# Kernel optimization log

Hardware: AMD Instinct MI355X
Metric: run time of the kernel (lower is better)

The kernel has to match this reference:

```python
import jax, jax.numpy as jnp
import numpy as np

B, DIM, HID = 16384, 1024, 2048
HALF = DIM // 2
# alternating checkerboard mask: even indices are 'masked' (conditioning) dims
_MASK = np.arange(DIM) % 2 == 0
MASK_IDX = np.nonzero(_MASK)[0]      # dims fed to the MLP (static)
NEG_IDX = np.nonzero(~_MASK)[0]      # dims transformed by the affine coupling (static)


def setup_inputs() -> dict:
    key = jax.random.key(0)
    ks = jax.random.split(key, 8)
    s = 0.02  # small init so exp(s) stays well-behaved
    return {
        "z": jax.random.normal(ks[0], (B, DIM), jnp.float32),
        "log_det": jnp.zeros((B,), jnp.float32),
        "W1": jax.random.normal(ks[1], (HID, HALF), jnp.float32) * s,
        "b1": jax.random.normal(ks[2], (HID,), jnp.float32) * s,
        "W2": jax.random.normal(ks[3], (HID, HID), jnp.float32) * s,
        "b2": jax.random.normal(ks[4], (HID,), jnp.float32) * s,
        "W3": jax.random.normal(ks[5], (DIM, HID), jnp.float32) * s,
        "b3": jax.random.normal(ks[6], (DIM,), jnp.float32) * s,
    }


def reference(z, log_det, W1, b1, W2, b2, W3, b3):
    # gather conditioning dims (static column indices -> jit-friendly)
    zm = z[:, MASK_IDX]                                    # [B, HALF]
    # 3-layer MLP with exact (erf) GELU, matching torch nn.GELU default
    h = jax.nn.gelu(zm @ W1.T + b1, approximate=False)     # [B, HID]
    h = jax.nn.gelu(h @ W2.T + b2, approximate=False)      # [B, HID]
    s_t = h @ W3.T + b3                                    # [B, DIM]
    s, t = s_t[:, :HALF], s_t[:, HALF:]                    # each [B, HALF]
    # affine coupling on the complementary dims, scatter back (forward, inverse=False)
    z_out = z.at[:, NEG_IDX].set(z[:, NEG_IDX] * jnp.exp(s) + t)
    log_det_out = log_det + jnp.sum(s, axis=1)
    return z_out, log_det_out
```

## Files before the change

### kernel.cpp

```cpp
#include <hip/hip_runtime.h>
#include <hip/hip_bf16.h>
#include <cstdint>

typedef __bf16 bf16x8 __attribute__((ext_vector_type(8)));
typedef float  f32x4  __attribute__((ext_vector_type(4)));

struct alignas(4) us2 { unsigned short x, y; };
struct alignas(8) us4 { unsigned short x, y, z, w; };

__device__ __forceinline__ unsigned short f2bf(float f) {
    union { float f; unsigned u; } a; a.f = f;
    unsigned r = a.u + 0x7fffu + ((a.u >> 16) & 1u);
    return (unsigned short)(r >> 16);
}

__device__ __forceinline__ void gl_lds16(const void* g, void* s) {
    __builtin_amdgcn_global_load_lds(
        (const __attribute__((address_space(1))) void*)g,
        (__attribute__((address_space(3))) void*)s, 16, 0, 0);
}

#define SCHEDB()  __builtin_amdgcn_sched_barrier(0)
#define SBAR()    do { SCHEDB(); __builtin_amdgcn_s_barrier(); SCHEDB(); } while (0)
#define WAITLG(N) do { asm volatile("s_waitcnt lgkmcnt(" #N ")" ::: "memory"); SCHEDB(); } while (0)
#define WAITVM(N) do { asm volatile("s_waitcnt vmcnt(" #N ")" ::: "memory"); SCHEDB(); } while (0)

template<int EPI, int K, int N>
__global__ __launch_bounds__(512, 2)
void gemm256(const unsigned short* __restrict__ A,
             const unsigned short* __restrict__ W,
             const float* __restrict__ bias,
             unsigned short* __restrict__ outb,
             float* __restrict__ outf,
             const float* __restrict__ zin,
             float* __restrict__ ldout)
{
    extern __shared__ char smem[];
    constexpr int NH = K / 32;
    constexpr int GX = N / 256;

    const int tid  = threadIdx.x;
    const int lane = tid & 63;
    const int wv   = tid >> 6;
    const int wr   = wv >> 2, wc = wv & 3;

    const int bid = blockIdx.y * GX + blockIdx.x;
    const int nwg = GX * (int)gridDim.y;
    const int swz = (bid & 7) * (nwg >> 3) + (bid >> 3);
    const size_t row0 = (size_t)(swz / GX) * 256;
    const size_t col0 = (size_t)(swz % GX) * 256;

    const int cse = (((tid & 3) ^ ((tid >> 3) & 3)) << 3);
    const unsigned short* ag = A + (row0 + (tid >> 2)) * (size_t)K + cse;
    const unsigned short* bg = W + (col0 + (tid >> 2)) * (size_t)K + cse;

    auto stage = [&](int hh) {
        char* dA = smem + (hh & 3) * 16384 + tid * 16;
        char* dB = dA + 65536;
        const unsigned short* a = ag + (size_t)hh * 32;
        const unsigned short* b = bg + (size_t)hh * 32;
        gl_lds16(a,                     dA);
        gl_lds16(a + (size_t)128 * K,   dA + 8192);
        gl_lds16(b,                     dB);
        gl_lds16(b + (size_t)128 * K,   dB + 8192);
    };

    const int ln15 = lane & 15;
    const int xo   = (((lane >> 4) ^ ((ln15 >> 1) & 3)) << 4);
    const int arow = wr * 128 + ln15;
    const int brow = wc * 64 + ln15;

#define LD(base, row) (*(const bf16x8*)((base) + (size_t)(row) * 64 + xo))

    f32x4 acc[8][4] = {};
    bf16x8 pA[4], pB[4], nA[4], nB[4], aH[4];

    stage(0); stage(1); stage(2);
    WAITVM(8);
    SBAR();
#pragma unroll
    for (int mf = 0; mf < 4; ++mf) pA[mf] = LD(smem, arow + mf * 16);
#pragma unroll
    for (int nf = 0; nf < 4; ++nf) pB[nf] = LD(smem + 65536, brow + nf * 16);

    for (int h = 0; h < NH; ++h) {
        const char* cA  = smem + (h & 3) * 16384;
        const char* cB  = cA + 65536;
        const char* cAn = smem + ((h + 1) & 3) * 16384;
        const char* cBn = cAn + 65536;

        if (h <= NH - 3) WAITVM(4);
        else             WAITVM(0);
        SBAR();

#pragma unroll
        for (int mf = 0; mf < 4; ++mf) aH[mf] = LD(cA, arow + 64 + mf * 16);
        WAITLG(4);
        __builtin_amdgcn_s_setprio(1);
#pragma unroll
        for (int mf = 0; mf < 4; ++mf)
#pragma unroll
            for (int nf = 0; nf < 4; ++nf)
                acc[mf][nf] = __builtin_amdgcn_mfma_f32_16x16x32_bf16(
                    pA[mf], pB[nf], acc[mf][nf], 0, 0, 0);
        __builtin_amdgcn_s_setprio(0);

        if (h + 1 < NH) {
#pragma unroll
            for (int mf = 0; mf < 4; ++mf) nA[mf] = LD(cAn, arow + mf * 16);
#pragma unroll
            for (int nf = 0; nf < 4; ++nf) nB[nf] = LD(cBn, brow + nf * 16);
            SCHEDB();
        }
        if (h + 3 < NH) stage(h + 3);

        if (h + 1 < NH) WAITLG(8);
        else            WAITLG(0);
        __builtin_amdgcn_s_setprio(1);
#pragma unroll
        for (int mf = 0; mf < 4; ++mf)
#pragma unroll
            for (int nf = 0; nf < 4; ++nf)
                acc[mf + 4][nf] = __builtin_amdgcn_mfma_f32_16x16x32_bf16(
                    aH[mf], pB[nf], acc[mf + 4][nf], 0, 0, 0);
        __builtin_amdgcn_s_setprio(0);

#pragma unroll
        for (int i = 0; i < 4; ++i) { pA[i] = nA[i]; pB[i] = nB[i]; }
    }
#undef LD

    const int lq = lane >> 4;
    float bv[4];
#pragma unroll
    for (int nf = 0; nf < 4; ++nf) bv[nf] = bias[col0 + wc * 64 + nf * 16 + ln15];

    if (EPI == 2) {
        const float2* zin2 = (const float2*)zin;
        float2*       out2 = (float2*)outf;
#pragma unroll
        for (int mi = 0; mi < 8; ++mi) {
#pragma unroll
            for (int r = 0; r < 4; ++r) {
                const size_t row = row0 + wr * 128 + mi * 16 + lq * 4 + r;
                float sv = 0.f;
#pragma unroll
                for (int p = 0; p < 2; ++p) {
                    float s = acc[mi][2 * p][r] + bv[2 * p];
                    float t = acc[mi][2 * p + 1][r] + bv[2 * p + 1];
                    const size_t j = (col0 >> 1) + wc * 32 + p * 16 + ln15;
                    float2 zv = zin2[row * 512 + j];
                    float2 o; o.x = zv.x; o.y = zv.y * __expf(s) + t;
                    out2[row * 512 + j] = o;
                    sv += s;
                }
                sv += __shfl_xor(sv, 1, 64);
                sv += __shfl_xor(sv, 2, 64);
                sv += __shfl_xor(sv, 4, 64);
                sv += __shfl_xor(sv, 8, 64);
                if (ln15 == 0) atomicAdd(&ldout[row], sv);
            }
        }
    } else {
#pragma unroll
        for (int mi = 0; mi < 8; ++mi) {
#pragma unroll
            for (int r = 0; r < 4; ++r) {
                const size_t row = row0 + wr * 128 + mi * 16 + lq * 4 + r;
#pragma unroll
                for (int nf = 0; nf < 4; ++nf) {
                    const size_t col = col0 + wc * 64 + nf * 16 + ln15;
                    float v = acc[mi][nf][r] + bv[nf];
                    if (EPI == 0) {
                        float g = 0.5f * v * (1.0f + erff(v * 0.70710678118654752f));
                        outb[row * N + col] = f2bf(g);
                    } else {
                        outf[row * N + col] = v;
                    }
                }
            }
        }
    }
}

__global__ void prep_all(const float* __restrict__ W1, const float* __restrict__ W2,
                         const float* __restrict__ W3, const float* __restrict__ b3,
                         const float* __restrict__ z,  const float* __restrict__ ld,
                         unsigned short* __restrict__ w1b, unsigned short* __restrict__ w2b,
                         unsigned short* __restrict__ w3i, float* __restrict__ b3i,
                         unsigned short* __restrict__ zm,  float* __restrict__ ldout)
{
    constexpr int N1 = 2048 * 512 / 4;
    constexpr int N2 = 2048 * 2048 / 4;
    constexpr int N3 = 1024 * 2048 / 4;
    constexpr int N4 = 16384 * 1024 / 4;
    constexpr int N5 = 1024;
    constexpr int N6 = 16384;
    constexpr int TOT = N1 + N2 + N3 + N4 + N5 + N6;
    const int stride = gridDim.x * blockDim.x;
    for (int i = blockIdx.x * blockDim.x + threadIdx.x; i < TOT; i += stride) {
        int j = i;
        if (j < N1) {
            float4 v = ((const float4*)W1)[j];
            ((us4*)w1b)[j] = us4{ f2bf(v.x), f2bf(v.y), f2bf(v.z), f2bf(v.w) };
            continue;
        }
        j -= N1;
        if (j < N2) {
            float4 v = ((const float4*)W2)[j];
            ((us4*)w2b)[j] = us4{ f2bf(v.x), f2bf(v.y), f2bf(v.z), f2bf(v.w) };
            continue;
        }
        j -= N2;
        if (j < N3) {
            int row = j >> 9, c4 = j & 511;
            int q = row >> 5, u = row & 31;
            int srcrow = (u < 16) ? (q * 16 + u) : (512 + q * 16 + u - 16);
            float4 v = ((const float4*)W3)[(size_t)srcrow * 512 + c4];
            ((us4*)w3i)[j] = us4{ f2bf(v.x), f2bf(v.y), f2bf(v.z), f2bf(v.w) };
            continue;
        }
        j -= N3;
        if (j < N4) {
            float4 v = ((const float4*)z)[j];
            ((us2*)zm)[j] = us2{ f2bf(v.x), f2bf(v.z) };
            continue;
        }
        j -= N4;
        if (j < N5) {
            int q = j >> 5, u = j & 31;
            b3i[j] = b3[(u < 16) ? (q * 16 + u) : (512 + q * 16 + u - 16)];
            continue;
        }
        j -= N5;
        ldout[j] = ld[j];
    }
}

extern "C" void kernel_launch(void* const* d_in, const int* in_sizes, int n_in,
                              void* d_out, int out_size, void* d_ws, size_t ws_size,
                              hipStream_t stream)
{
    const float* z  = (const float*)d_in[0];
    const float* ld = (const float*)d_in[1];
    const float* W1 = (const float*)d_in[2];
    const float* b1 = (const float*)d_in[3];
    const float* W2 = (const float*)d_in[4];
    const float* b2 = (const float*)d_in[5];
    const float* W3 = (const float*)d_in[6];
    const float* b3 = (const float*)d_in[7];

    float* out   = (float*)d_out;
    float* zout  = out;
    float* ldout = out + (size_t)16384 * 1024;

    char* w = (char*)d_ws;
    unsigned short* zm  = (unsigned short*)w; w += (size_t)16384 * 512 * 2;
    unsigned short* w1b = (unsigned short*)w; w += (size_t)2048 * 512 * 2;
    unsigned short* w2b = (unsigned short*)w; w += (size_t)2048 * 2048 * 2;
    unsigned short* w3i = (unsigned short*)w; w += (size_t)1024 * 2048 * 2;
    unsigned short* h1  = (unsigned short*)w; w += (size_t)16384 * 2048 * 2;
    unsigned short* h2  = (unsigned short*)w; w += (size_t)16384 * 2048 * 2;
    float*          b3i = (float*)w;          w += 1024 * 4;

    (void)hipFuncSetAttribute((const void*)&gemm256<0, 512,  2048>,
                              hipFuncAttributeMaxDynamicSharedMemorySize, 131072);
    (void)hipFuncSetAttribute((const void*)&gemm256<0, 2048, 2048>,
                              hipFuncAttributeMaxDynamicSharedMemorySize, 131072);
    (void)hipFuncSetAttribute((const void*)&gemm256<2, 2048, 1024>,
                              hipFuncAttributeMaxDynamicSharedMemorySize, 131072);

    prep_all<<<2048, 256, 0, stream>>>(W1, W2, W3, b3, z, ld,
                                       w1b, w2b, w3i, b3i, zm, ldout);

    gemm256<0, 512,  2048><<<dim3(8, 64), 512, 131072, stream>>>(zm, w1b, b1, h1, nullptr, nullptr, nullptr);
    gemm256<0, 2048, 2048><<<dim3(8, 64), 512, 131072, stream>>>(h1, w2b, b2, h2, nullptr, nullptr, nullptr);
    gemm256<2, 2048, 1024><<<dim3(4, 64), 512, 131072, stream>>>(h2, w3i, b3i, nullptr, zout, z, ldout);
}
```

Measured before the change: 317.1 us.

## Restructure GEMM main loop into two barrier-separated phases with split A/B staging

Rewrites the K-loop pipeline of the bf16 MFMA GEMM. The register-level double buffering of the next tile's fragments (pA/pB/nA/nB) is removed. Each iteration now loads its current fragments from LDS, issues the A global-to-LDS prefetch in the first half and the B prefetch in the second half, and separates the phases with extra barriers. The intent is to cut register pressure and spread the global loads across the iteration. The cost is more s_barriers and full lgkmcnt waits before each MFMA block, which exposes LDS read latency that was previously hidden.

```diff
diff --git a/kernel.cpp b/kernel.cpp
--- a/kernel.cpp
+++ b/kernel.cpp
@@ -54,15 +54,17 @@
     const unsigned short* ag = A + (row0 + (tid >> 2)) * (size_t)K + cse;
     const unsigned short* bg = W + (col0 + (tid >> 2)) * (size_t)K + cse;
 
-    auto stage = [&](int hh) {
+    auto stage_a = [&](int hh) {
         char* dA = smem + (hh & 3) * 16384 + tid * 16;
-        char* dB = dA + 65536;
         const unsigned short* a = ag + (size_t)hh * 32;
+        gl_lds16(a,                   dA);
+        gl_lds16(a + (size_t)128 * K, dA + 8192);
+    };
+    auto stage_b = [&](int hh) {
+        char* dB = smem + (hh & 3) * 16384 + 65536 + tid * 16;
         const unsigned short* b = bg + (size_t)hh * 32;
-        gl_lds16(a,                     dA);
-        gl_lds16(a + (size_t)128 * K,   dA + 8192);
-        gl_lds16(b,                     dB);
-        gl_lds16(b + (size_t)128 * K,   dB + 8192);
+        gl_lds16(b,                   dB);
+        gl_lds16(b + (size_t)128 * K, dB + 8192);
     };
 
     const int ln15 = lane & 15;
@@ -73,60 +75,52 @@
 #define LD(base, row) (*(const bf16x8*)((base) + (size_t)(row) * 64 + xo))
 
     f32x4 acc[8][4] = {};
-    bf16x8 pA[4], pB[4], nA[4], nB[4], aH[4];
-
-    stage(0); stage(1); stage(2);
+
+    stage_a(0); stage_b(0);
+    stage_a(1); stage_b(1);
+    stage_a(2); stage_b(2);
     WAITVM(8);
     SBAR();
-#pragma unroll
-    for (int mf = 0; mf < 4; ++mf) pA[mf] = LD(smem, arow + mf * 16);
-#pragma unroll
-    for (int nf = 0; nf < 4; ++nf) pB[nf] = LD(smem + 65536, brow + nf * 16);
 
     for (int h = 0; h < NH; ++h) {
-        const char* cA  = smem + (h & 3) * 16384;
-        const char* cB  = cA + 65536;
-        const char* cAn = smem + ((h + 1) & 3) * 16384;
-        const char* cBn = cAn + 65536;
-
-        if (h <= NH - 3) WAITVM(4);
-        else             WAITVM(0);
-        SBAR();
-
-#pragma unroll
-        for (int mf = 0; mf < 4; ++mf) aH[mf] = LD(cA, arow + 64 + mf * 16);
-        WAITLG(4);
+        const char* cA = smem + (h & 3) * 16384;
+        const char* cB = cA + 65536;
+        bf16x8 aL[4], aH[4], bF[4];
+
+#pragma unroll
+        for (int mf = 0; mf < 4; ++mf) aL[mf] = LD(cA, arow + mf * 16);
+#pragma unroll
+        for (int nf = 0; nf < 4; ++nf) bF[nf] = LD(cB, brow + nf * 16);
+        if (h + 3 < NH) stage_a(h + 3);
+        SBAR();
+        WAITLG(0);
         __builtin_amdgcn_s_setprio(1);
 #pragma unroll
         for (int mf = 0; mf < 4; ++mf)
 #pragma unroll
             for (int nf = 0; nf < 4; ++nf)
                 acc[mf][nf] = __builtin_amdgcn_mfma_f32_16x16x32_bf16(
-                    pA[mf], pB[nf], acc[mf][nf], 0, 0, 0);
+                    aL[mf], bF[nf], acc[mf][nf], 0, 0, 0);
         __builtin_amdgcn_s_setprio(0);
-
-        if (h + 1 < NH) {
-#pragma unroll
-            for (int mf = 0; mf < 4; ++mf) nA[mf] = LD(cAn, arow + mf * 16);
-#pragma unroll
-            for (int nf = 0; nf < 4; ++nf) nB[nf] = LD(cBn, brow + nf * 16);
-            SCHEDB();
-        }
-        if (h + 3 < NH) stage(h + 3);
-
-        if (h + 1 < NH) WAITLG(8);
-        else            WAITLG(0);
+        SBAR();
+
+#pragma unroll
+        for (int mf = 0; mf < 4; ++mf) aH[mf] = LD(cA, arow + 64 + mf * 16);
+        if (h + 3 < NH) stage_b(h + 3);
+        if (h < NH - 3)       WAITVM(8);
+        else if (h == NH - 3) WAITVM(4);
+        else if (h == NH - 2) WAITVM(0);
+        SBAR();
+        WAITLG(0);
         __builtin_amdgcn_s_setprio(1);
 #pragma unroll
         for (int mf = 0; mf < 4; ++mf)
 #pragma unroll
             for (int nf = 0; nf < 4; ++nf)
                 acc[mf + 4][nf] = __builtin_amdgcn_mfma_f32_16x16x32_bf16(
-                    aH[mf], pB[nf], acc[mf + 4][nf], 0, 0, 0);
+                    aH[mf], bF[nf], acc[mf + 4][nf], 0, 0, 0);
         __builtin_amdgcn_s_setprio(0);
-
-#pragma unroll
-        for (int i = 0; i < 4; ++i) { pA[i] = nA[i]; pB[i] = nB[i]; }
+        SBAR();
     }
 #undef LD
 
```

Measured after the change: 327.4 us. 1.03x slower.

## Unfuse affine coupling epilogue from final GEMM into separate finalize kernel

Applied to the files above, without the earlier changes.

The final GEMM no longer applies the coupling in its epilogue. It now writes raw s/t fp32 output to a scratch buffer that reuses h1, using an un-interleaved W3. A new finalize2 kernel reads s, t and z row by row with float4 loads, writes z_out, and computes log_det by a per-row warp reduction instead of atomics. This removes the strided float2 epilogue, the atomics and the prep-time W3/b3 interleaving, at the cost of an extra 64MB fp32 write and read round trip plus one more kernel launch.

```diff
diff --git a/kernel.cpp b/kernel.cpp
--- a/kernel.cpp
+++ b/kernel.cpp
@@ -31,9 +31,7 @@
              const unsigned short* __restrict__ W,
              const float* __restrict__ bias,
              unsigned short* __restrict__ outb,
-             float* __restrict__ outf,
-             const float* __restrict__ zin,
-             float* __restrict__ ldout)
+             float* __restrict__ outf)
 {
     extern __shared__ char smem[];
     constexpr int NH = K / 32;
@@ -85,7 +83,6 @@
 
     for (int h = 0; h < NH; ++h) {
         const char* cA  = smem + (h & 3) * 16384;
-        const char* cB  = cA + 65536;
         const char* cAn = smem + ((h + 1) & 3) * 16384;
         const char* cBn = cAn + 65536;
 
@@ -135,68 +132,73 @@
 #pragma unroll
     for (int nf = 0; nf < 4; ++nf) bv[nf] = bias[col0 + wc * 64 + nf * 16 + ln15];
 
-    if (EPI == 2) {
-        const float2* zin2 = (const float2*)zin;
-        float2*       out2 = (float2*)outf;
-#pragma unroll
-        for (int mi = 0; mi < 8; ++mi) {
-#pragma unroll
-            for (int r = 0; r < 4; ++r) {
-                const size_t row = row0 + wr * 128 + mi * 16 + lq * 4 + r;
-                float sv = 0.f;
-#pragma unroll
-                for (int p = 0; p < 2; ++p) {
-                    float s = acc[mi][2 * p][r] + bv[2 * p];
-                    float t = acc[mi][2 * p + 1][r] + bv[2 * p + 1];
-                    const size_t j = (col0 >> 1) + wc * 32 + p * 16 + ln15;
-                    float2 zv = zin2[row * 512 + j];
-                    float2 o; o.x = zv.x; o.y = zv.y * __expf(s) + t;
-                    out2[row * 512 + j] = o;
-                    sv += s;
-                }
-                sv += __shfl_xor(sv, 1, 64);
-                sv += __shfl_xor(sv, 2, 64);
-                sv += __shfl_xor(sv, 4, 64);
-                sv += __shfl_xor(sv, 8, 64);
-                if (ln15 == 0) atomicAdd(&ldout[row], sv);
-            }
-        }
-    } else {
-#pragma unroll
-        for (int mi = 0; mi < 8; ++mi) {
-#pragma unroll
-            for (int r = 0; r < 4; ++r) {
-                const size_t row = row0 + wr * 128 + mi * 16 + lq * 4 + r;
-#pragma unroll
-                for (int nf = 0; nf < 4; ++nf) {
-                    const size_t col = col0 + wc * 64 + nf * 16 + ln15;
-                    float v = acc[mi][nf][r] + bv[nf];
-                    if (EPI == 0) {
-                        float g = 0.5f * v * (1.0f + erff(v * 0.70710678118654752f));
-                        outb[row * N + col] = f2bf(g);
-                    } else {
-                        outf[row * N + col] = v;
-                    }
+#pragma unroll
+    for (int mi = 0; mi < 8; ++mi) {
+#pragma unroll
+        for (int r = 0; r < 4; ++r) {
+            const size_t row = row0 + wr * 128 + mi * 16 + lq * 4 + r;
+#pragma unroll
+            for (int nf = 0; nf < 4; ++nf) {
+                const size_t col = col0 + wc * 64 + nf * 16 + ln15;
+                float v = acc[mi][nf][r] + bv[nf];
+                if (EPI == 0) {
+                    float g = 0.5f * v * (1.0f + erff(v * 0.70710678118654752f));
+                    outb[row * N + col] = f2bf(g);
+                } else {
+                    outf[row * N + col] = v;
                 }
             }
         }
     }
 }
 
+__global__ __launch_bounds__(256)
+void finalize2(const float* __restrict__ st, const float* __restrict__ z,
+               const float* __restrict__ ld, float* __restrict__ zout,
+               float* __restrict__ ldout)
+{
+    const int lane = threadIdx.x & 63;
+    const int wvi  = threadIdx.x >> 6;
+    const int rb   = blockIdx.x * 8 + wvi * 2;
+#pragma unroll
+    for (int rr = 0; rr < 2; ++rr) {
+        const int row = rb + rr;
+        const float4* s4p = (const float4*)(st + (size_t)row * 1024);
+        const float4* t4p = (const float4*)(st + (size_t)row * 1024 + 512);
+        const float4* z4p = (const float4*)(z  + (size_t)row * 1024);
+        float4*       o4p = (float4*)(zout + (size_t)row * 1024);
+        float lsum = 0.f;
+#pragma unroll
+        for (int half = 0; half < 2; ++half) {
+            const int i = lane + half * 64;
+            float4 s = s4p[i];
+            float4 t = t4p[i];
+            float4 z0 = z4p[2 * i], z1 = z4p[2 * i + 1];
+            float4 o0, o1;
+            o0.x = z0.x; o0.y = z0.y * __expf(s.x) + t.x;
+            o0.z = z0.z; o0.w = z0.w * __expf(s.y) + t.y;
+            o1.x = z1.x; o1.y = z1.y * __expf(s.z) + t.z;
+            o1.z = z1.z; o1.w = z1.w * __expf(s.w) + t.w;
+            o4p[2 * i]     = o0;
+            o4p[2 * i + 1] = o1;
+            lsum += s.x + s.y + s.z + s.w;
+        }
+#pragma unroll
+        for (int off = 32; off > 0; off >>= 1) lsum += __shfl_down(lsum, off, 64);
+        if (lane == 0) ldout[row] = ld[row] + lsum;
+    }
+}
+
 __global__ void prep_all(const float* __restrict__ W1, const float* __restrict__ W2,
-                         const float* __restrict__ W3, const float* __restrict__ b3,
-                         const float* __restrict__ z,  const float* __restrict__ ld,
+                         const float* __restrict__ W3, const float* __restrict__ z,
                          unsigned short* __restrict__ w1b, unsigned short* __restrict__ w2b,
-                         unsigned short* __restrict__ w3i, float* __restrict__ b3i,
-                         unsigned short* __restrict__ zm,  float* __restrict__ ldout)
+                         unsigned short* __restrict__ w3b, unsigned short* __restrict__ zm)
 {
     constexpr int N1 = 2048 * 512 / 4;
     constexpr int N2 = 2048 * 2048 / 4;
     constexpr int N3 = 1024 * 2048 / 4;
     constexpr int N4 = 16384 * 1024 / 4;
-    constexpr int N5 = 1024;
-    constexpr int N6 = 16384;
-    constexpr int TOT = N1 + N2 + N3 + N4 + N5 + N6;
+    constexpr int TOT = N1 + N2 + N3 + N4;
     const int stride = gridDim.x * blockDim.x;
     for (int i = blockIdx.x * blockDim.x + threadIdx.x; i < TOT; i += stride) {
         int j = i;
@@ -213,27 +215,13 @@
         }
         j -= N2;
         if (j < N3) {
-            int row = j >> 9, c4 = j & 511;
-            int q = row >> 5, u = row & 31;
-            int srcrow = (u < 16) ? (q * 16 + u) : (512 + q * 16 + u - 16);
-            float4 v = ((const float4*)W3)[(size_t)srcrow * 512 + c4];
-            ((us4*)w3i)[j] = us4{ f2bf(v.x), f2bf(v.y), f2bf(v.z), f2bf(v.w) };
+            float4 v = ((const float4*)W3)[j];
+            ((us4*)w3b)[j] = us4{ f2bf(v.x), f2bf(v.y), f2bf(v.z), f2bf(v.w) };
             continue;
         }
         j -= N3;
-        if (j < N4) {
-            float4 v = ((const float4*)z)[j];
-            ((us2*)zm)[j] = us2{ f2bf(v.x), f2bf(v.z) };
-            continue;
-        }
-        j -= N4;
-        if (j < N5) {
-            int q = j >> 5, u = j & 31;
-            b3i[j] = b3[(u < 16) ? (q * 16 + u) : (512 + q * 16 + u - 16)];
-            continue;
-        }
-        j -= N5;
-        ldout[j] = ld[j];
+        float4 v = ((const float4*)z)[j];
+        ((us2*)zm)[j] = us2{ f2bf(v.x), f2bf(v.z) };
     }
 }
 
@@ -258,22 +246,23 @@
     unsigned short* zm  = (unsigned short*)w; w += (size_t)16384 * 512 * 2;
     unsigned short* w1b = (unsigned short*)w; w += (size_t)2048 * 512 * 2;
     unsigned short* w2b = (unsigned short*)w; w += (size_t)2048 * 2048 * 2;
-    unsigned short* w3i = (unsigned short*)w; w += (size_t)1024 * 2048 * 2;
+    unsigned short* w3b = (unsigned short*)w; w += (size_t)1024 * 2048 * 2;
     unsigned short* h1  = (unsigned short*)w; w += (size_t)16384 * 2048 * 2;
     unsigned short* h2  = (unsigned short*)w; w += (size_t)16384 * 2048 * 2;
-    float*          b3i = (float*)w;          w += 1024 * 4;
+    float* st = (float*)h1;
 
     (void)hipFuncSetAttribute((const void*)&gemm256<0, 512,  2048>,
                               hipFuncAttributeMaxDynamicSharedMemorySize, 131072);
     (void)hipFuncSetAttribute((const void*)&gemm256<0, 2048, 2048>,
                               hipFuncAttributeMaxDynamicSharedMemorySize, 131072);
-    (void)hipFuncSetAttribute((const void*)&gemm256<2, 2048, 1024>,
+    (void)hipFuncSetAttribute((const void*)&gemm256<1, 2048, 1024>,
                               hipFuncAttributeMaxDynamicSharedMemorySize, 131072);
 
-    prep_all<<<2048, 256, 0, stream>>>(W1, W2, W3, b3, z, ld,
-                                       w1b, w2b, w3i, b3i, zm, ldout);
-
-    gemm256<0, 512,  2048><<<dim3(8, 64), 512, 131072, stream>>>(zm, w1b, b1, h1, nullptr, nullptr, nullptr);
-    gemm256<0, 2048, 2048><<<dim3(8, 64), 512, 131072, stream>>>(h1, w2b, b2, h2, nullptr, nullptr, nullptr);
-    gemm256<2, 2048, 1024><<<dim3(4, 64), 512, 131072, stream>>>(h2, w3i, b3i, nullptr, zout, z, ldout);
-}
+    prep_all<<<2048, 256, 0, stream>>>(W1, W2, W3, z, w1b, w2b, w3b, zm);
+
+    gemm256<0, 512,  2048><<<dim3(8, 64), 512, 131072, stream>>>(zm, w1b, b1, h1, nullptr);
+    gemm256<0, 2048, 2048><<<dim3(8, 64), 512, 131072, stream>>>(h1, w2b, b2, h2, nullptr);
+    gemm256<1, 2048, 1024><<<dim3(4, 64), 512, 131072, stream>>>(h2, w3b, b3, nullptr, st);
+
+    finalize2<<<2048, 256, 0, stream>>>(st, z, ld, zout, ldout);
+}
```

Measured after the change: 330.3 us. 1.04x slower.

## Shrink GEMM tiles to 256x128 with 4 waves and 3-stage LDS ring

Applied to the files above, without the earlier changes.

The bf16 GEMM kernels go from 256x256 tiles with 8 waves to 256x128 tiles with 4 waves per block, doubling the grid. LDS drops to 72KB with a 3-slot ring buffer for A and B. All fragments for a k-step are loaded from LDS at once instead of being software-pipelined across iterations. The aim is more blocks per CU and better load balance across the device. The cost is lower data reuse per tile and less overlap between LDS reads and MFMA work.

```diff
diff --git a/kernel.cpp b/kernel.cpp
--- a/kernel.cpp
+++ b/kernel.cpp
@@ -26,7 +26,7 @@
 #define WAITVM(N) do { asm volatile("s_waitcnt vmcnt(" #N ")" ::: "memory"); SCHEDB(); } while (0)
 
 template<int EPI, int K, int N>
-__global__ __launch_bounds__(512, 2)
+__global__ __launch_bounds__(256, 2)
 void gemm256(const unsigned short* __restrict__ A,
              const unsigned short* __restrict__ W,
              const float* __restrict__ bias,
@@ -37,32 +37,34 @@
 {
     extern __shared__ char smem[];
     constexpr int NH = K / 32;
-    constexpr int GX = N / 256;
+    constexpr int GX = N / 128;
 
     const int tid  = threadIdx.x;
     const int lane = tid & 63;
     const int wv   = tid >> 6;
-    const int wr   = wv >> 2, wc = wv & 3;
+    const int wr   = wv >> 1, wc = wv & 1;
 
     const int bid = blockIdx.y * GX + blockIdx.x;
     const int nwg = GX * (int)gridDim.y;
     const int swz = (bid & 7) * (nwg >> 3) + (bid >> 3);
     const size_t row0 = (size_t)(swz / GX) * 256;
-    const size_t col0 = (size_t)(swz % GX) * 256;
+    const size_t col0 = (size_t)(swz % GX) * 128;
 
     const int cse = (((tid & 3) ^ ((tid >> 3) & 3)) << 3);
     const unsigned short* ag = A + (row0 + (tid >> 2)) * (size_t)K + cse;
     const unsigned short* bg = W + (col0 + (tid >> 2)) * (size_t)K + cse;
 
-    auto stage = [&](int hh) {
-        char* dA = smem + (hh & 3) * 16384 + tid * 16;
-        char* dB = dA + 65536;
+    auto stage = [&](int hh, int sl) {
+        char* dA = smem + sl * 16384 + tid * 16;
+        char* dB = smem + 49152 + sl * 8192 + tid * 16;
         const unsigned short* a = ag + (size_t)hh * 32;
         const unsigned short* b = bg + (size_t)hh * 32;
-        gl_lds16(a,                     dA);
-        gl_lds16(a + (size_t)128 * K,   dA + 8192);
-        gl_lds16(b,                     dB);
-        gl_lds16(b + (size_t)128 * K,   dB + 8192);
+        gl_lds16(a,                    dA);
+        gl_lds16(a + (size_t) 64 * K,  dA + 4096);
+        gl_lds16(a + (size_t)128 * K,  dA + 8192);
+        gl_lds16(a + (size_t)192 * K,  dA + 12288);
+        gl_lds16(b,                    dB);
+        gl_lds16(b + (size_t) 64 * K,  dB + 4096);
     };
 
     const int ln15 = lane & 15;
@@ -70,31 +72,33 @@
     const int arow = wr * 128 + ln15;
     const int brow = wc * 64 + ln15;
 
-#define LD(base, row) (*(const bf16x8*)((base) + (size_t)(row) * 64 + xo))
+#define LDA(sl, row) (*(const bf16x8*)(smem + (sl) * 16384 + (size_t)(row) * 64 + xo))
+#define LDB(sl, row) (*(const bf16x8*)(smem + 49152 + (sl) * 8192 + (size_t)(row) * 64 + xo))
 
     f32x4 acc[8][4] = {};
-    bf16x8 pA[4], pB[4], nA[4], nB[4], aH[4];
-
-    stage(0); stage(1); stage(2);
-    WAITVM(8);
-    SBAR();
-#pragma unroll
-    for (int mf = 0; mf < 4; ++mf) pA[mf] = LD(smem, arow + mf * 16);
-#pragma unroll
-    for (int nf = 0; nf < 4; ++nf) pB[nf] = LD(smem + 65536, brow + nf * 16);
-
+
+    stage(0, 0); stage(1, 1);
+
+    int sl = 0;
     for (int h = 0; h < NH; ++h) {
-        const char* cA  = smem + (h & 3) * 16384;
-        const char* cB  = cA + 65536;
-        const char* cAn = smem + ((h + 1) & 3) * 16384;
-        const char* cBn = cAn + 65536;
-
-        if (h <= NH - 3) WAITVM(4);
-        else             WAITVM(0);
+        if (h < NH - 1) WAITVM(6);
+        else            WAITVM(0);
         SBAR();
 
-#pragma unroll
-        for (int mf = 0; mf < 4; ++mf) aH[mf] = LD(cA, arow + 64 + mf * 16);
+        bf16x8 aF[8], bF[4];
+#pragma unroll
+        for (int mf = 0; mf < 4; ++mf) aF[mf] = LDA(sl, arow + mf * 16);
+#pragma unroll
+        for (int nf = 0; nf < 4; ++nf) bF[nf] = LDB(sl, brow + nf * 16);
+        SCHEDB();
+#pragma unroll
+        for (int mf = 4; mf < 8; ++mf) aF[mf] = LDA(sl, arow + mf * 16);
+        SCHEDB();
+        {
+            int sl2 = sl + 2; if (sl2 >= 3) sl2 -= 3;
+            if (h + 2 < NH) stage(h + 2, sl2);
+        }
+
         WAITLG(4);
         __builtin_amdgcn_s_setprio(1);
 #pragma unroll
@@ -102,33 +106,23 @@
 #pragma unroll
             for (int nf = 0; nf < 4; ++nf)
                 acc[mf][nf] = __builtin_amdgcn_mfma_f32_16x16x32_bf16(
-                    pA[mf], pB[nf], acc[mf][nf], 0, 0, 0);
+                    aF[mf], bF[nf], acc[mf][nf], 0, 0, 0);
         __builtin_amdgcn_s_setprio(0);
 
-        if (h + 1 < NH) {
-#pragma unroll
-            for (int mf = 0; mf < 4; ++mf) nA[mf] = LD(cAn, arow + mf * 16);
-#pragma unroll
-            for (int nf = 0; nf < 4; ++nf) nB[nf] = LD(cBn, brow + nf * 16);
-            SCHEDB();
-        }
-        if (h + 3 < NH) stage(h + 3);
-
-        if (h + 1 < NH) WAITLG(8);
-        else            WAITLG(0);
+        WAITLG(0);
         __builtin_amdgcn_s_setprio(1);
 #pragma unroll
-        for (int mf = 0; mf < 4; ++mf)
+        for (int mf = 4; mf < 8; ++mf)
 #pragma unroll
             for (int nf = 0; nf < 4; ++nf)
-                acc[mf + 4][nf] = __builtin_amdgcn_mfma_f32_16x16x32_bf16(
-                    aH[mf], pB[nf], acc[mf + 4][nf], 0, 0, 0);
+                acc[mf][nf] = __builtin_amdgcn_mfma_f32_16x16x32_bf16(
+                    aF[mf], bF[nf], acc[mf][nf], 0, 0, 0);
         __builtin_amdgcn_s_setprio(0);
 
-#pragma unroll
-        for (int i = 0; i < 4; ++i) { pA[i] = nA[i]; pB[i] = nB[i]; }
+        ++sl; if (sl == 3) sl = 0;
     }
-#undef LD
+#undef LDA
+#undef LDB
 
     const int lq = lane >> 4;
     float bv[4];
@@ -264,16 +258,16 @@
     float*          b3i = (float*)w;          w += 1024 * 4;
 
     (void)hipFuncSetAttribute((const void*)&gemm256<0, 512,  2048>,
-                              hipFuncAttributeMaxDynamicSharedMemorySize, 131072);
+                              hipFuncAttributeMaxDynamicSharedMemorySize, 73728);
     (void)hipFuncSetAttribute((const void*)&gemm256<0, 2048, 2048>,
-                              hipFuncAttributeMaxDynamicSharedMemorySize, 131072);
+                              hipFuncAttributeMaxDynamicSharedMemorySize, 73728);
     (void)hipFuncSetAttribute((const void*)&gemm256<2, 2048, 1024>,
-                              hipFuncAttributeMaxDynamicSharedMemorySize, 131072);
+                              hipFuncAttributeMaxDynamicSharedMemorySize, 73728);
 
     prep_all<<<2048, 256, 0, stream>>>(W1, W2, W3, b3, z, ld,
                                        w1b, w2b, w3i, b3i, zm, ldout);
 
-    gemm256<0, 512,  2048><<<dim3(8, 64), 512, 131072, stream>>>(zm, w1b, b1, h1, nullptr, nullptr, nullptr);
-    gemm256<0, 2048, 2048><<<dim3(8, 64), 512, 131072, stream>>>(h1, w2b, b2, h2, nullptr, nullptr, nullptr);
-    gemm256<2, 2048, 1024><<<dim3(4, 64), 512, 131072, stream>>>(h2, w3i, b3i, nullptr, zout, z, ldout);
-}
+    gemm256<0, 512,  2048><<<dim3(16, 64), 256, 73728, stream>>>(zm, w1b, b1, h1, nullptr, nullptr, nullptr);
+    gemm256<0, 2048, 2048><<<dim3(16, 64), 256, 73728, stream>>>(h1, w2b, b2, h2, nullptr, nullptr, nullptr);
+    gemm256<2, 2048, 1024><<<dim3(8, 64),  256, 73728, stream>>>(h2, w3i, b3i, nullptr, zout, z, ldout);
+}
```

Result: slower. 342.6 us (+8.0%).
